# Kernel optimization log

Measured on AMD Instinct MI355X. Metric: run time of the kernel, lower is better.

The kernel has to match this reference:

```python
import jax, jax.numpy as jnp
import numpy as np

NUM_HEADS = 16
NEG_INF = -1e9


def setup_inputs() -> dict:
    key = jax.random.key(0)
    ks = jax.random.split(key, 12)
    T, B, E = 2048, 4, 1024
    s = 0.02
    inp = {
        "query": jax.random.normal(ks[0], (T, B, E), jnp.float32),
        "key": jax.random.normal(ks[1], (T, B, E), jnp.float32),
        "value": jax.random.normal(ks[2], (T, B, E), jnp.float32),
        # causal additive mask [T, S]: 0 on/below diagonal, -1e9 above
        "attn_mask": jnp.where(
            jnp.arange(T)[:, None] >= jnp.arange(T)[None, :], 0.0, NEG_INF
        ).astype(jnp.float32),
        "wq": jax.random.normal(ks[3], (E, E), jnp.float32) * s,
        "bq": jax.random.normal(ks[4], (E,), jnp.float32) * s,
        "wk": jax.random.normal(ks[5], (E, E), jnp.float32) * s,
        "bk": jax.random.normal(ks[6], (E,), jnp.float32) * s,
        "wv": jax.random.normal(ks[7], (E, E), jnp.float32) * s,
        "bv": jax.random.normal(ks[8], (E,), jnp.float32) * s,
        "wo": jax.random.normal(ks[9], (E, E), jnp.float32) * s,
        "bo": jax.random.normal(ks[10], (E,), jnp.float32) * s,
    }
    return inp


def reference(query, key, value, attn_mask, wq, bq, wk, bk, wv, bv, wo, bo):
    T, B, E = query.shape
    H = NUM_HEADS
    D = E // H
    scaling = D ** (-0.5)
    # projections (torch Linear: x @ W.T + b)
    q = (query @ wq.T + bq) * scaling          # [T, B, E]
    k = key @ wk.T + bk                         # [S, B, E]
    v = value @ wv.T + bv                       # [S, B, E]
    # -> [B*H, len, D]
    q = q.reshape(T, B * H, D).transpose(1, 0, 2)
    k = k.reshape(-1, B * H, D).transpose(1, 0, 2)
    v = v.reshape(-1, B * H, D).transpose(1, 0, 2)
    # scores [B*H, T, S], additive mask, softmax (dropout = identity in eval)
    attn_weights = jnp.einsum('ntd,nsd->nts', q, k) + attn_mask
    attn_weights = jax.nn.softmax(attn_weights, axis=-1)
    attn = jnp.einsum('nts,nsd->ntd', attn_weights, v)   # [B*H, T, D]
    attn = attn.transpose(1, 0, 2).reshape(T, B, E)
    return attn @ wo.T + bo
```

## Files before the change

kernel.cpp:

```cpp
#include <hip/hip_runtime.h>
#include <hip/hip_bf16.h>

typedef __hip_bfloat16 bf16;
typedef __attribute__((ext_vector_type(8))) short short8;
typedef __attribute__((ext_vector_type(4))) float float4v;

#define TLEN  2048
#define BATCH 4
#define EMB   1024
#define HEADS 16
#define HD    64
#define MROWS (TLEN*BATCH)
#define PSTRIDE 72
#define SMAX2 5.770780f
#define QSCALE 0.18033688f

__device__ __forceinline__ void gl2lds16(const bf16* g, bf16* l) {
    __builtin_amdgcn_global_load_lds(
        (const __attribute__((address_space(1))) void*)g,
        (__attribute__((address_space(3))) void*)l, 16, 0, 0);
}

__device__ __forceinline__ void store_out(float* p, float v)  { *p = v; }
__device__ __forceinline__ void store_out(bf16* p, float v)   { *p = __float2bfloat16(v); }

__device__ __forceinline__ void cvt8(const float* __restrict__ src,
                                     bf16* __restrict__ dst, int t) {
    const float4v a = ((const float4v*)src)[2*t];
    const float4v b = ((const float4v*)src)[2*t + 1];
    union { short8 v; bf16 h[8]; } u;
    u.h[0] = __float2bfloat16(a[0]);
    u.h[1] = __float2bfloat16(a[1]);
    u.h[2] = __float2bfloat16(a[2]);
    u.h[3] = __float2bfloat16(a[3]);
    u.h[4] = __float2bfloat16(b[0]);
    u.h[5] = __float2bfloat16(b[1]);
    u.h[6] = __float2bfloat16(b[2]);
    u.h[7] = __float2bfloat16(b[3]);
    ((short8*)dst)[t] = u.v;
}

__global__ __launch_bounds__(256)
void cvt_act(const float* __restrict__ s0, const float* __restrict__ s1,
             const float* __restrict__ s2, bf16* __restrict__ d0,
             bf16* __restrict__ d1, bf16* __restrict__ d2, int n8)
{
    const int t = blockIdx.x * 256 + threadIdx.x;
    if (t >= n8) return;
    const float* s = blockIdx.y == 0 ? s0 : (blockIdx.y == 1 ? s1 : s2);
    bf16*        d = blockIdx.y == 0 ? d0 : (blockIdx.y == 1 ? d1 : d2);
    cvt8(s, d, t);
}

__global__ __launch_bounds__(256)
void cvt_wt(const float* __restrict__ s0, const float* __restrict__ s1,
            const float* __restrict__ s2, const float* __restrict__ s3,
            bf16* __restrict__ d0, bf16* __restrict__ d1,
            bf16* __restrict__ d2, bf16* __restrict__ d3, int n8)
{
    const int t = blockIdx.x * 256 + threadIdx.x;
    if (t >= n8) return;
    const float* s = blockIdx.y == 0 ? s0 : (blockIdx.y == 1 ? s1 :
                     (blockIdx.y == 2 ? s2 : s3));
    bf16*        d = blockIdx.y == 0 ? d0 : (blockIdx.y == 1 ? d1 :
                     (blockIdx.y == 2 ? d2 : d3));
    cvt8(s, d, t);
}

template<typename OutT>
__device__ __forceinline__ void gemm_body(
    const bf16* __restrict__ A, const bf16* __restrict__ Bw,
    const float* __restrict__ bias, OutT* __restrict__ out,
    float scale, int mode, int bm_i, int bn_i)
{
    __shared__ __align__(16) bf16 As[128*32];
    __shared__ __align__(16) bf16 Bs[128*32];
    const int tid  = threadIdx.x;
    const int lane = tid & 63;
    const int wave = tid >> 6;
    const int wm   = (wave >> 1) * 64;
    const int wn   = (wave & 1) * 64;
    const int quad = lane >> 4;
    const int l16  = lane & 15;
    const size_t bm = bm_i;
    const size_t bn = bn_i;

    const bf16* Ag = A  + bm*128*(size_t)EMB + (size_t)(tid>>2)*EMB + (tid&3)*8;
    const bf16* Bg = Bw + bn*128*(size_t)EMB + (size_t)(tid>>2)*EMB + (tid&3)*8;
    bf16* Al = As + tid*8;
    bf16* Bl = Bs + tid*8;

    float4v acc[4][4];
    #pragma unroll
    for (int i=0;i<4;i++)
        #pragma unroll
        for (int j=0;j<4;j++) acc[i][j] = (float4v){0.f,0.f,0.f,0.f};

    for (int k0 = 0; k0 < EMB; k0 += 32) {
        __syncthreads();
        gl2lds16(Ag + k0,                   Al);
        gl2lds16(Ag + 64*(size_t)EMB + k0,  Al + 64*32);
        gl2lds16(Bg + k0,                   Bl);
        gl2lds16(Bg + 64*(size_t)EMB + k0,  Bl + 64*32);
        __syncthreads();

        short8 af[4], bfr[4];
        #pragma unroll
        for (int i=0;i<4;i++)
            af[i] = *(const short8*)(As + (wm + i*16 + l16)*32 + quad*8);
        #pragma unroll
        for (int j=0;j<4;j++)
            bfr[j] = *(const short8*)(Bs + (wn + j*16 + l16)*32 + quad*8);
        #pragma unroll
        for (int i=0;i<4;i++)
            #pragma unroll
            for (int j=0;j<4;j++)
                acc[i][j] = __builtin_amdgcn_mfma_f32_16x16x32_bf16(
                                af[i], bfr[j], acc[i][j], 0, 0, 0);
    }

    #pragma unroll
    for (int i=0;i<4;i++) {
        #pragma unroll
        for (int j=0;j<4;j++) {
            const int n = (int)bn*128 + wn + j*16 + l16;
            const float bf = bias[n];
            #pragma unroll
            for (int r=0;r<4;r++) {
                const int m = (int)bm*128 + wm + i*16 + quad*4 + r;
                const float v = (acc[i][j][r] + bf) * scale;
                size_t idx;
                if (mode == 0) {
                    idx = (size_t)m*EMB + n;
                } else {
                    const int t = m >> 2, b = m & 3;
                    const int h = n >> 6, d = n & 63;
                    if (mode == 1) idx = (((size_t)(b*HEADS + h))*TLEN + t)*HD + d;
                    else           idx = (((size_t)(b*HEADS + h))*HD + d)*TLEN + t;
                }
                store_out(out + idx, v);
            }
        }
    }
}

__global__ __launch_bounds__(256, 2)
void gemm_qkv(const bf16* __restrict__ xq, const bf16* __restrict__ xk,
              const bf16* __restrict__ xv,
              const bf16* __restrict__ wq, const bf16* __restrict__ wk,
              const bf16* __restrict__ wv,
              const float* __restrict__ bq, const float* __restrict__ bk,
              const float* __restrict__ bv,
              bf16* __restrict__ oq, bf16* __restrict__ ok,
              bf16* __restrict__ ov)
{
    const int id  = blockIdx.x;
    const int xcd = id & 7;
    const int r   = id >> 3;
    const int z   = r >> 6;
    const int rem = r & 63;
    const int bm  = xcd + 8*(rem >> 3);
    const int bn  = rem & 7;

    const bf16*  A  = z == 0 ? xq : (z == 1 ? xk : xv);
    const bf16*  W  = z == 0 ? wq : (z == 1 ? wk : wv);
    const float* bi = z == 0 ? bq : (z == 1 ? bk : bv);
    bf16*        o  = z == 0 ? oq : (z == 1 ? ok : ov);
    const float  sc = z == 0 ? QSCALE : 1.0f;
    const int    md = z == 2 ? 2 : 1;
    gemm_body<bf16>(A, W, bi, o, sc, md, bm, bn);
}

__global__ __launch_bounds__(256, 2)
void gemm_out(const bf16* __restrict__ A, const bf16* __restrict__ W,
              const float* __restrict__ bias, float* __restrict__ out)
{
    const int id  = blockIdx.x;
    const int xcd = id & 7;
    const int r   = id >> 3;
    const int bm  = xcd + 8*(r >> 3);
    const int bn  = r & 7;
    gemm_body<float>(A, W, bias, out, 1.0f, 0, bm, bn);
}

__global__ __launch_bounds__(256, 2)
void flash_attn(const bf16* __restrict__ Q, const bf16* __restrict__ K,
                const bf16* __restrict__ Vt, bf16* __restrict__ Aout)
{
    __shared__ __align__(16) bf16 Ks[2][64*64];
    __shared__ __align__(16) bf16 Vs[2][64*64];
    __shared__ __align__(16) bf16 Ps[4*32*PSTRIDE];
    const int tid  = threadIdx.x;
    const int lane = tid & 63;
    const int wave = tid >> 6;
    const int quad = lane >> 4;
    const int l16  = lane & 15;

    const int id  = blockIdx.x;
    const int xcd = id & 7;
    const int jj  = id >> 3;
    const int bh  = xcd + 8*(jj & 7);
    const int tq  = 15 - (jj >> 3);
    const int qbase = tq*128 + wave*32;

    short8 qf[2][2];
    #pragma unroll
    for (int f=0; f<2; f++) {
        const bf16* qrow = Q + ((size_t)bh*TLEN + qbase + f*16 + l16)*HD;
        qf[f][0] = *(const short8*)(qrow + quad*8);
        qf[f][1] = *(const short8*)(qrow + 32 + quad*8);
    }

    float4v o[2][4];
    float lsum[2][4];
    #pragma unroll
    for (int f=0; f<2; f++)
        #pragma unroll
        for (int j=0;j<4;j++) { o[f][j] = (float4v){0.f,0.f,0.f,0.f}; }
    #pragma unroll
    for (int f=0; f<2; f++)
        #pragma unroll
        for (int r=0;r<4;r++) lsum[f][r] = 0.f;

    bf16* Pw = Ps + wave*32*PSTRIDE;

    const int srow   = tid >> 3;
    const int schunk = (tid & 7) ^ (srow & 7);
    const bf16* Kg = K  + (size_t)bh*TLEN*HD + (size_t)srow*HD   + schunk*8;
    const bf16* Vg = Vt + (size_t)bh*HD*TLEN + (size_t)srow*TLEN + schunk*8;
    const int ldst = tid*8;

    const int nt = 2*tq + 2;
    gl2lds16(Kg,           &Ks[0][ldst]);
    gl2lds16(Kg + 32*HD,   &Ks[0][32*64 + ldst]);
    gl2lds16(Vg,           &Vs[0][ldst]);
    gl2lds16(Vg + 32*TLEN, &Vs[0][32*64 + ldst]);

    for (int i = 0; i < nt; i++) {
        const int buf = i & 1;
        __syncthreads();
        if (i + 1 < nt) {
            const int nb = buf ^ 1;
            const size_t s0n = (size_t)(i+1)*64;
            gl2lds16(Kg + s0n*HD,        &Ks[nb][ldst]);
            gl2lds16(Kg + (s0n+32)*HD,   &Ks[nb][32*64 + ldst]);
            gl2lds16(Vg + s0n,           &Vs[nb][ldst]);
            gl2lds16(Vg + 32*TLEN + s0n, &Vs[nb][32*64 + ldst]);
        }

        float4v scr[2][4];
        #pragma unroll
        for (int f=0; f<2; f++)
            #pragma unroll
            for (int j=0;j<4;j++) scr[f][j] = (float4v){0.f,0.f,0.f,0.f};
        #pragma unroll
        for (int h2=0; h2<2; h2++) {
            const int psw = ((h2<<2) | quad) ^ (l16 & 7);
            #pragma unroll
            for (int j=0;j<4;j++) {
                short8 kf = *(const short8*)(&Ks[buf][(j*16 + l16)*64 + psw*8]);
                scr[0][j] = __builtin_amdgcn_mfma_f32_16x16x32_bf16(qf[0][h2], kf, scr[0][j], 0,0,0);
                scr[1][j] = __builtin_amdgcn_mfma_f32_16x16x32_bf16(qf[1][h2], kf, scr[1][j], 0,0,0);
            }
        }

        #pragma unroll
        for (int f=0; f<2; f++) {
            const bool needmask = (i*64 + 63) > (qbase + f*16);
            if (needmask) {
                #pragma unroll
                for (int j=0;j<4;j++)
                    #pragma unroll
                    for (int r=0;r<4;r++) {
                        const int t = qbase + f*16 + quad*4 + r;
                        const int s = i*64 + j*16 + l16;
                        const float p = (s <= t) ? exp2f(scr[f][j][r] - SMAX2) : 0.f;
                        lsum[f][r] += p;
                        Pw[(f*16 + quad*4 + r)*PSTRIDE + j*16 + l16] = __float2bfloat16(p);
                    }
            } else {
                #pragma unroll
                for (int j=0;j<4;j++)
                    #pragma unroll
                    for (int r=0;r<4;r++) {
                        const float p = exp2f(scr[f][j][r] - SMAX2);
                        lsum[f][r] += p;
                        Pw[(f*16 + quad*4 + r)*PSTRIDE + j*16 + l16] = __float2bfloat16(p);
                    }
            }
        }

        #pragma unroll
        for (int h2=0; h2<2; h2++) {
            const int psw = ((h2<<2) | quad) ^ (l16 & 7);
            short8 pf0 = *(const short8*)(Pw + (l16)*PSTRIDE      + h2*32 + quad*8);
            short8 pf1 = *(const short8*)(Pw + (16 + l16)*PSTRIDE + h2*32 + quad*8);
            #pragma unroll
            for (int j=0;j<4;j++) {
                short8 vf = *(const short8*)(&Vs[buf][(j*16 + l16)*64 + psw*8]);
                o[0][j] = __builtin_amdgcn_mfma_f32_16x16x32_bf16(pf0, vf, o[0][j], 0,0,0);
                o[1][j] = __builtin_amdgcn_mfma_f32_16x16x32_bf16(pf1, vf, o[1][j], 0,0,0);
            }
        }
    }

    #pragma unroll
    for (int f=0; f<2; f++)
        #pragma unroll
        for (int r=0;r<4;r++) {
            float s = lsum[f][r];
            #pragma unroll
            for (int off=1; off<16; off<<=1) s += __shfl_xor(s, off);
            lsum[f][r] = s;
        }
    const int b = bh >> 4, h = bh & 15;
    #pragma unroll
    for (int f=0; f<2; f++)
        #pragma unroll
        for (int j=0;j<4;j++)
            #pragma unroll
            for (int r=0;r<4;r++) {
                const int t = qbase + f*16 + quad*4 + r;
                const int d = j*16 + l16;
                const float v = o[f][j][r] / lsum[f][r];
                Aout[((size_t)t*BATCH + b)*EMB + h*64 + d] = __float2bfloat16(v);
            }
}

extern "C" void kernel_launch(void* const* d_in, const int* in_sizes, int n_in,
                              void* d_out, int out_size, void* d_ws, size_t ws_size,
                              hipStream_t stream)
{
    const float* query = (const float*)d_in[0];
    const float* key   = (const float*)d_in[1];
    const float* value = (const float*)d_in[2];
    const float* wq = (const float*)d_in[4];
    const float* bq = (const float*)d_in[5];
    const float* wk = (const float*)d_in[6];
    const float* bk = (const float*)d_in[7];
    const float* wv = (const float*)d_in[8];
    const float* bv = (const float*)d_in[9];
    const float* wo = (const float*)d_in[10];
    const float* bo = (const float*)d_in[11];

    const size_t actsz = (size_t)MROWS*EMB;
    const size_t wsz   = (size_t)EMB*EMB;
    bf16* xq    = (bf16*)d_ws;
    bf16* xk    = xq  + actsz;
    bf16* xv    = xk  + actsz;
    bf16* wqb   = xv  + actsz;
    bf16* wkb   = wqb + wsz;
    bf16* wvb   = wkb + wsz;
    bf16* wob   = wvb + wsz;
    bf16* q_ws  = wob + wsz;
    bf16* k_ws  = q_ws + actsz;
    bf16* v_ws  = k_ws + actsz;

    const dim3 blk(256);

    hipLaunchKernelGGL(cvt_act, dim3((int)(actsz/8/256), 3), blk, 0, stream,
                       query, key, value, xq, xk, xv, (int)(actsz/8));
    hipLaunchKernelGGL(cvt_wt, dim3((int)(wsz/8/256), 4), blk, 0, stream,
                       wq, wk, wv, wo, wqb, wkb, wvb, wob, (int)(wsz/8));

    hipLaunchKernelGGL(gemm_qkv, dim3(1536), blk, 0, stream,
                       xq, xk, xv, wqb, wkb, wvb, bq, bk, bv, q_ws, k_ws, v_ws);

    hipLaunchKernelGGL(flash_attn, dim3(1024), blk, 0, stream, q_ws, k_ws, v_ws, xq);

    hipLaunchKernelGGL(gemm_out, dim3(512), blk, 0, stream, xq, wob, bo, (float*)d_out);
}
```

Measured before the change: 345.3 us.

## Deepen GEMM K-tile to 64 with swizzled LDS and transpose V output via LDS

The GEMM main loop now loads 64-wide K slices per iteration into an XOR-swizzled LDS layout. This halves the number of barrier pairs and avoids LDS bank conflicts on the fragment reads. The transposed V projection output (mode 2) is staged through shared memory so each lane writes 16-byte contiguous chunks along T, replacing the strided scalar stores. The two conversion kernels are merged into one launch. LDS use per block doubles, which may lower occupancy.

```diff
diff --git a/kernel.cpp b/kernel.cpp
--- a/kernel.cpp
+++ b/kernel.cpp
@@ -4,6 +4,7 @@
 typedef __hip_bfloat16 bf16;
 typedef __attribute__((ext_vector_type(8))) short short8;
 typedef __attribute__((ext_vector_type(4))) float float4v;
+typedef __attribute__((ext_vector_type(2))) unsigned long long ull2;
 
 #define TLEN  2048
 #define BATCH 4
@@ -41,40 +42,39 @@
 }
 
 __global__ __launch_bounds__(256)
-void cvt_act(const float* __restrict__ s0, const float* __restrict__ s1,
-             const float* __restrict__ s2, bf16* __restrict__ d0,
-             bf16* __restrict__ d1, bf16* __restrict__ d2, int n8)
-{
-    const int t = blockIdx.x * 256 + threadIdx.x;
-    if (t >= n8) return;
-    const float* s = blockIdx.y == 0 ? s0 : (blockIdx.y == 1 ? s1 : s2);
-    bf16*        d = blockIdx.y == 0 ? d0 : (blockIdx.y == 1 ? d1 : d2);
-    cvt8(s, d, t);
-}
-
-__global__ __launch_bounds__(256)
-void cvt_wt(const float* __restrict__ s0, const float* __restrict__ s1,
-            const float* __restrict__ s2, const float* __restrict__ s3,
-            bf16* __restrict__ d0, bf16* __restrict__ d1,
-            bf16* __restrict__ d2, bf16* __restrict__ d3, int n8)
-{
-    const int t = blockIdx.x * 256 + threadIdx.x;
-    if (t >= n8) return;
-    const float* s = blockIdx.y == 0 ? s0 : (blockIdx.y == 1 ? s1 :
-                     (blockIdx.y == 2 ? s2 : s3));
-    bf16*        d = blockIdx.y == 0 ? d0 : (blockIdx.y == 1 ? d1 :
-                     (blockIdx.y == 2 ? d2 : d3));
-    cvt8(s, d, t);
+void cvt_all(const float* __restrict__ q, const float* __restrict__ k,
+             const float* __restrict__ v,
+             const float* __restrict__ wq, const float* __restrict__ wk,
+             const float* __restrict__ wv, const float* __restrict__ wo,
+             bf16* __restrict__ xq, bf16* __restrict__ xk, bf16* __restrict__ xv,
+             bf16* __restrict__ wqb, bf16* __restrict__ wkb,
+             bf16* __restrict__ wvb, bf16* __restrict__ wob)
+{
+    const int id = blockIdx.x * 256 + threadIdx.x;
+    const int NA = 1 << 20, NW = 1 << 17;
+    if (id < 3*NA) {
+        const int w = id >> 20, off = id & (NA - 1);
+        const float* s = w == 0 ? q : (w == 1 ? k : v);
+        bf16*        d = w == 0 ? xq : (w == 1 ? xk : xv);
+        cvt8(s, d, off);
+    } else {
+        const int id2 = id - 3*NA;
+        const int w = id2 >> 17, off = id2 & (NW - 1);
+        const float* s = w == 0 ? wq : (w == 1 ? wk : (w == 2 ? wv : wo));
+        bf16*        d = w == 0 ? wqb : (w == 1 ? wkb : (w == 2 ? wvb : wob));
+        cvt8(s, d, off);
+    }
 }
 
 template<typename OutT>
 __device__ __forceinline__ void gemm_body(
     const bf16* __restrict__ A, const bf16* __restrict__ Bw,
     const float* __restrict__ bias, OutT* __restrict__ out,
-    float scale, int mode, int bm_i, int bn_i)
-{
-    __shared__ __align__(16) bf16 As[128*32];
-    __shared__ __align__(16) bf16 Bs[128*32];
+    float scale, int mode, int bm, int bn)
+{
+    __shared__ __align__(16) bf16 smem[128*64*2];
+    bf16* As = smem;
+    bf16* Bs = smem + 128*64;
     const int tid  = threadIdx.x;
     const int lane = tid & 63;
     const int wave = tid >> 6;
@@ -82,11 +82,12 @@
     const int wn   = (wave & 1) * 64;
     const int quad = lane >> 4;
     const int l16  = lane & 15;
-    const size_t bm = bm_i;
-    const size_t bn = bn_i;
-
-    const bf16* Ag = A  + bm*128*(size_t)EMB + (size_t)(tid>>2)*EMB + (tid&3)*8;
-    const bf16* Bg = Bw + bn*128*(size_t)EMB + (size_t)(tid>>2)*EMB + (tid&3)*8;
+    const int hl   = wn >> 6;
+
+    const int srow = tid >> 3;
+    const int skc  = (tid & 7) ^ (srow & 7);
+    const bf16* Ag = A  + (size_t)(bm*128 + srow)*EMB + skc*8;
+    const bf16* Bg = Bw + (size_t)(bn*128 + srow)*EMB + skc*8;
     bf16* Al = As + tid*8;
     bf16* Bl = Bs + tid*8;
 
@@ -96,50 +97,92 @@
         #pragma unroll
         for (int j=0;j<4;j++) acc[i][j] = (float4v){0.f,0.f,0.f,0.f};
 
-    for (int k0 = 0; k0 < EMB; k0 += 32) {
+    for (int k0 = 0; k0 < EMB; k0 += 64) {
         __syncthreads();
-        gl2lds16(Ag + k0,                   Al);
-        gl2lds16(Ag + 64*(size_t)EMB + k0,  Al + 64*32);
-        gl2lds16(Bg + k0,                   Bl);
-        gl2lds16(Bg + 64*(size_t)EMB + k0,  Bl + 64*32);
+        #pragma unroll
+        for (int g=0; g<4; g++) {
+            gl2lds16(Ag + (size_t)g*32*EMB + k0, Al + g*2048);
+            gl2lds16(Bg + (size_t)g*32*EMB + k0, Bl + g*2048);
+        }
         __syncthreads();
 
-        short8 af[4], bfr[4];
-        #pragma unroll
-        for (int i=0;i<4;i++)
-            af[i] = *(const short8*)(As + (wm + i*16 + l16)*32 + quad*8);
-        #pragma unroll
-        for (int j=0;j<4;j++)
-            bfr[j] = *(const short8*)(Bs + (wn + j*16 + l16)*32 + quad*8);
-        #pragma unroll
-        for (int i=0;i<4;i++)
+        #pragma unroll
+        for (int half=0; half<2; half++) {
+            const int pc = (((half<<2) | quad) ^ (l16 & 7)) * 8;
+            short8 af[4], bfr[4];
+            #pragma unroll
+            for (int i=0;i<4;i++)
+                af[i] = *(const short8*)(As + (wm + i*16 + l16)*64 + pc);
             #pragma unroll
             for (int j=0;j<4;j++)
-                acc[i][j] = __builtin_amdgcn_mfma_f32_16x16x32_bf16(
-                                af[i], bfr[j], acc[i][j], 0, 0, 0);
+                bfr[j] = *(const short8*)(Bs + (wn + j*16 + l16)*64 + pc);
+            #pragma unroll
+            for (int i=0;i<4;i++)
+                #pragma unroll
+                for (int j=0;j<4;j++)
+                    acc[i][j] = __builtin_amdgcn_mfma_f32_16x16x32_bf16(
+                                    af[i], bfr[j], acc[i][j], 0, 0, 0);
+        }
     }
 
-    #pragma unroll
-    for (int i=0;i<4;i++) {
-        #pragma unroll
-        for (int j=0;j<4;j++) {
-            const int n = (int)bn*128 + wn + j*16 + l16;
-            const float bf = bias[n];
-            #pragma unroll
-            for (int r=0;r<4;r++) {
-                const int m = (int)bm*128 + wm + i*16 + quad*4 + r;
-                const float v = (acc[i][j][r] + bf) * scale;
-                size_t idx;
-                if (mode == 0) {
-                    idx = (size_t)m*EMB + n;
-                } else {
-                    const int t = m >> 2, b = m & 3;
-                    const int h = n >> 6, d = n & 63;
-                    if (mode == 1) idx = (((size_t)(b*HEADS + h))*TLEN + t)*HD + d;
-                    else           idx = (((size_t)(b*HEADS + h))*HD + d)*TLEN + t;
+    if (mode != 2) {
+        #pragma unroll
+        for (int i=0;i<4;i++) {
+            #pragma unroll
+            for (int j=0;j<4;j++) {
+                const int n = bn*128 + wn + j*16 + l16;
+                const float bf = bias[n];
+                #pragma unroll
+                for (int r=0;r<4;r++) {
+                    const int m = bm*128 + wm + i*16 + quad*4 + r;
+                    const float v = (acc[i][j][r] + bf) * scale;
+                    size_t idx;
+                    if (mode == 0) {
+                        idx = (size_t)m*EMB + n;
+                    } else {
+                        const int t = m >> 2, b = m & 3;
+                        const int h = n >> 6, d = n & 63;
+                        idx = (((size_t)(b*HEADS + h))*TLEN + t)*HD + d;
+                    }
+                    store_out(out + idx, v);
                 }
-                store_out(out + idx, v);
-            }
+            }
+        }
+    } else {
+        __syncthreads();
+        bf16* Tb = smem;
+        #pragma unroll
+        for (int i=0;i<4;i++) {
+            const int tc = (wm >> 4) + i;
+            #pragma unroll
+            for (int j=0;j<4;j++) {
+                const int d = j*16 + l16;
+                const float bf = bias[bn*128 + wn + d];
+                #pragma unroll
+                for (int r=0;r<4;r++) {
+                    const float v = acc[i][j][r] + bf;
+                    Tb[((((r<<1)|hl)*64 + d) << 5) + ((tc ^ (d & 7)) << 2) + quad]
+                        = __float2bfloat16(v);
+                }
+            }
+        }
+        __syncthreads();
+        bf16* ob = (bf16*)out;
+        #pragma unroll
+        for (int pass=0; pass<8; pass++) {
+            const int row = pass*64 + (tid >> 2);
+            const int c16 = tid & 3;
+            const int b2  = row >> 7;
+            const int h2l = (row >> 6) & 1;
+            const int d   = row & 63;
+            const int e   = d & 7;
+            const unsigned long long lo =
+                *(const unsigned long long*)(Tb + (row << 5) + ((( (2*c16)   ^ e) << 2)));
+            const unsigned long long hi =
+                *(const unsigned long long*)(Tb + (row << 5) + ((( (2*c16+1) ^ e) << 2)));
+            ull2 val; val.x = lo; val.y = hi;
+            *(ull2*)(ob + ((size_t)((b2*HEADS + bn*2 + h2l)*HD + d))*TLEN
+                        + bm*32 + c16*8) = val;
         }
     }
 }
@@ -358,10 +401,9 @@
 
     const dim3 blk(256);
 
-    hipLaunchKernelGGL(cvt_act, dim3((int)(actsz/8/256), 3), blk, 0, stream,
-                       query, key, value, xq, xk, xv, (int)(actsz/8));
-    hipLaunchKernelGGL(cvt_wt, dim3((int)(wsz/8/256), 4), blk, 0, stream,
-                       wq, wk, wv, wo, wqb, wkb, wvb, wob, (int)(wsz/8));
+    hipLaunchKernelGGL(cvt_all, dim3(14336), blk, 0, stream,
+                       query, key, value, wq, wk, wv, wo,
+                       xq, xk, xv, wqb, wkb, wvb, wob);
 
     hipLaunchKernelGGL(gemm_qkv, dim3(1536), blk, 0, stream,
                        xq, xk, xv, wqb, wkb, wvb, bq, bk, bv, q_ws, k_ws, v_ws);
```

Result: faster. 317.0 us (-8.2%).
